# Kernel tuning notes

Measured on AMD Instinct MI355X. Metric: run time of the kernel, lower is better.

Reference implementation:

```python
import jax, jax.numpy as jnp
import numpy as np

N_PROT, N_SUB = 50000, 2000
D_PROT, D_SUB, D_PROJ, KERNEL, N_INT = 256, 256, 128, 16, 64


def setup_inputs() -> dict:
    key = jax.random.key(0)
    ks = jax.random.split(key, 8)
    init = lambda k, shape: jax.random.normal(k, shape, dtype=jnp.float32) * 0.02
    return {
        "prot_node": jax.random.normal(ks[0], (N_PROT, D_PROT), dtype=jnp.float32),
        "sub_node": jax.random.normal(ks[1], (N_SUB, D_SUB), dtype=jnp.float32),
        "int_index": jax.random.randint(ks[2], (N_INT,), 0, N_SUB),
        "Wp": init(ks[3], (D_PROT, D_PROJ)),  # prot_proj weight (in,out layout)
        "bp": jnp.zeros((D_PROJ,), jnp.float32),
        "Ws": init(ks[4], (D_SUB, D_PROJ)),   # sub_proj weight
        "bs": jnp.zeros((D_PROJ,), jnp.float32),
        "wa": init(ks[5], (2 * D_PROJ,)),     # attention_proj weight (out dim 1)
        "ba": jnp.zeros((), jnp.float32),
        "sub_out": init(ks[6], (D_PROJ, D_SUB)),
        "prot_out": init(ks[7], (D_PROJ, D_PROT)),
    }


def reference(prot_node, sub_node, int_index, Wp, bp, Ws, bs, wa, ba, sub_out, prot_out):
    K = KERNEL
    prot_proj = prot_node @ Wp + bp                              # [N, D]
    # reaction potion: sum of projected interacting substrate nodes -> [D]
    reaction = jnp.sum(sub_node[int_index] @ Ws + bs, axis=0)
    num_windows = prot_node.shape[0] - K + 1                     # W
    # attention_proj(concat(window_row, reaction)) splits linearly:
    #   logit = window_row . wa[:D] + reaction . wa[D:] + ba
    # The reaction part is a per-row constant -> compute per-node logits once.
    w1, w2 = wa[:D_PROJ], wa[D_PROJ:]
    g = prot_proj @ w1 + (reaction @ w2 + ba)                    # [N]
    # sliding-window gather indices [W, K]
    idx = jnp.arange(num_windows)[:, None] + jnp.arange(K)[None, :]
    attn = jax.nn.softmax(g[idx], axis=1)                        # [W, K] softmax over window
    local = jnp.einsum('wk,wkd->wd', attn, prot_proj[idx])       # [W, D]
    scores = local + reaction                                    # [W, D]
    # rank windows and pick the best
    top = jnp.argmax(jnp.sum(scores, axis=1))
    top_score = scores[top]                                      # [D]
    # scatter updates back into the node features
    # (set matches torch's non-accumulating fancy-index += for duplicate indices;
    #  the added delta is identical for every row anyway)
    sub_new = sub_node.at[int_index].set(sub_node[int_index] + top_score @ sub_out)
    prot_delta = top_score @ prot_out                            # [D_PROT]
    win = jax.lax.dynamic_slice(prot_node, (top, 0), (K, D_PROT))
    prot_new = jax.lax.dynamic_update_slice(prot_node, win + prot_delta, (top, 0))
    return prot_new, sub_new, int_index
```

## Files before the change

kernel.cpp:

```cpp
#include <hip/hip_runtime.h>
#include <math.h>

#define N_PROT 50000
#define N_SUB  2000
#define D_PROT 256
#define D_SUB  256
#define D_PROJ 128
#define KW     16
#define N_INT  64
#define NWIN   (N_PROT - KW + 1)

#define OUT_SUB (N_PROT * D_PROT)
#define OUT_IDX (OUT_SUB + N_SUB * D_SUB)

#define WS_PACK  0
#define WS_REACT 2
#define WS_CNT   130
#define WS_U1    132
#define WS_U2    388
#define WS_G     644
#define WS_P     (WS_G + N_PROT)

#define PB 1563
#define SB 64
#define NBLK (PB + SB)
#define WBLK ((NWIN + 255) / 256)

__global__ __launch_bounds__(256) void k_prep(
    const float* __restrict__ sub_node, const int* __restrict__ int_index,
    const float* __restrict__ Ws, const float* __restrict__ bs,
    const float* __restrict__ Wp, const float* __restrict__ wa,
    float* __restrict__ ws) {
  const int tid = threadIdx.x;
  if (blockIdx.x == 0) {
    __shared__ int   sidx[N_INT];
    __shared__ float ssum[D_SUB];
    if (tid < N_INT) sidx[tid] = int_index[tid];
    __syncthreads();
    float acc = 0.f;
    #pragma unroll 8
    for (int i = 0; i < N_INT; ++i) acc += sub_node[sidx[i] * D_SUB + tid];
    ssum[tid] = acc;
    __syncthreads();
    if (tid < D_PROJ) {
      float r = 64.0f * bs[tid];
      #pragma unroll 8
      for (int d = 0; d < D_SUB; ++d) r = fmaf(ssum[d], Ws[d * D_PROJ + tid], r);
      ws[WS_REACT + tid] = r;
    }
    if (tid == 0) {
      *((unsigned long long*)ws) = 0ull;
      ((unsigned int*)ws)[WS_CNT] = 0u;
    }
  } else {
    __shared__ float swa[D_PROJ];
    if (tid < D_PROJ) swa[tid] = wa[tid];
    __syncthreads();
    float s1 = 0.f, s2 = 0.f;
    const float4* wrow = (const float4*)&Wp[tid * D_PROJ];
    #pragma unroll 8
    for (int j4 = 0; j4 < D_PROJ / 4; ++j4) {
      float4 w = wrow[j4];
      float4 a = *(const float4*)&swa[j4 * 4];
      s1 = fmaf(w.x, a.x, fmaf(w.y, a.y, fmaf(w.z, a.z, fmaf(w.w, a.w, s1))));
      s2 += w.x + w.y + w.z + w.w;
    }
    ws[WS_U1 + tid] = s1;
    ws[WS_U2 + tid] = s2;
  }
}

__global__ __launch_bounds__(256) void k_main(
    const float* __restrict__ prot, const float* __restrict__ sub_node,
    const int* __restrict__ int_index, float* __restrict__ out,
    float* __restrict__ ws) {
  const int tid = threadIdx.x, lane = tid & 63, wave = tid >> 6;
  const int b = blockIdx.x;
  if (b < PB) {
    const float4 c1 = *(const float4*)&ws[WS_U1 + lane * 4];
    const float4 c2 = *(const float4*)&ws[WS_U2 + lane * 4];
    const int rbase = b * 32 + wave * 8;
    if (rbase + 8 <= N_PROT) {
      float4 av[8];
      #pragma unroll
      for (int i = 0; i < 8; ++i)
        av[i] = *(const float4*)&prot[(rbase + i) * D_PROT + lane * 4];
      #pragma unroll
      for (int i = 0; i < 8; ++i)
        *(float4*)&out[(rbase + i) * D_PROT + lane * 4] = av[i];
      #pragma unroll
      for (int i = 0; i < 8; ++i) {
        float g = av[i].x * c1.x + av[i].y * c1.y + av[i].z * c1.z + av[i].w * c1.w;
        float p = av[i].x * c2.x + av[i].y * c2.y + av[i].z * c2.z + av[i].w * c2.w;
        #pragma unroll
        for (int off = 32; off > 0; off >>= 1) {
          g += __shfl_xor(g, off, 64);
          p += __shfl_xor(p, off, 64);
        }
        if (lane == 0) {
          const int r = rbase + i;
          ws[WS_G + r] = g; ws[WS_P + r] = p;
        }
      }
    } else {
      for (int i = 0; i < 8; ++i) {
        const int r = rbase + i;
        if (r >= N_PROT) break;
        const float4 av = *(const float4*)&prot[r * D_PROT + lane * 4];
        *(float4*)&out[r * D_PROT + lane * 4] = av;
        float g = av.x * c1.x + av.y * c1.y + av.z * c1.z + av.w * c1.w;
        float p = av.x * c2.x + av.y * c2.y + av.z * c2.z + av.w * c2.w;
        for (int off = 32; off > 0; off >>= 1) {
          g += __shfl_xor(g, off, 64);
          p += __shfl_xor(p, off, 64);
        }
        if (lane == 0) { ws[WS_G + r] = g; ws[WS_P + r] = p; }
      }
    }
  } else {
    const int sb = b - PB;
    #pragma unroll
    for (int i = 0; i < 8; ++i) {
      const int gi = sb * 2048 + i * 256 + tid;
      if (gi < (N_SUB * D_SUB) / 4)
        *(float4*)&out[OUT_SUB + gi * 4] = *(const float4*)&sub_node[gi * 4];
    }
    if (sb == 0 && tid < N_INT) out[OUT_IDX + tid] = (float)int_index[tid];
  }
}

__global__ __launch_bounds__(256) void k_finish(
    const float* __restrict__ prot, const float* __restrict__ sub_node,
    const int* __restrict__ int_index, const float* __restrict__ Wp,
    const float* __restrict__ bp, const float* __restrict__ sub_out,
    const float* __restrict__ prot_out, float* __restrict__ ws,
    float* __restrict__ out) {
  __shared__ float sg[256 + KW], sp[256 + KW];
  __shared__ unsigned long long wred[4];
  __shared__ int slast;
  const int tid = threadIdx.x;
  const int w0 = blockIdx.x * 256;
  for (int i = tid; i < 256 + KW - 1; i += 256) {
    int idx = w0 + i;
    bool ok = idx < N_PROT;
    sg[i] = ok ? ws[WS_G + idx] : -1e30f;
    sp[i] = ok ? ws[WS_P + idx] : 0.f;
  }
  __syncthreads();
  {
    int w = w0 + tid;
    unsigned long long best = 0ull;
    if (w < NWIN) {
      float m = sg[tid];
      #pragma unroll
      for (int k = 1; k < KW; ++k) m = fmaxf(m, sg[tid + k]);
      float s = 0.f, t = 0.f;
      #pragma unroll
      for (int k = 0; k < KW; ++k) {
        float e = expf(sg[tid + k] - m);
        s += e;
        t = fmaf(e, sp[tid + k], t);
      }
      t /= s;
      unsigned int bb = __float_as_uint(t);
      unsigned int u = bb ^ ((bb & 0x80000000u) ? 0xFFFFFFFFu : 0x80000000u);
      best = ((unsigned long long)u << 32) |
             (unsigned long long)(0xFFFFFFFFu - (unsigned)w);
    }
    #pragma unroll
    for (int off = 32; off > 0; off >>= 1) {
      unsigned long long o = __shfl_xor(best, off, 64);
      if (o > best) best = o;
    }
    if ((tid & 63) == 0) wred[tid >> 6] = best;
  }
  __syncthreads();
  if (tid == 0) {
    unsigned long long b2 = wred[0];
    for (int i = 1; i < 4; ++i) if (wred[i] > b2) b2 = wred[i];
    atomicMax((unsigned long long*)ws, b2);
    __threadfence();
    unsigned int ticket = atomicAdd(&((unsigned int*)ws)[WS_CNT], 1u);
    slast = (ticket == WBLK - 1) ? 1 : 0;
  }
  __syncthreads();
  if (!slast) return;

  __shared__ float aprot[KW][D_PROT];
  __shared__ float proj16[KW][D_PROJ];
  __shared__ float attn[KW];
  __shared__ float ts[D_PROJ];
  __shared__ float pdelta[D_PROT], sdelta[D_SUB];
  __shared__ int   sidx[N_INT];
  __shared__ int   swtop;
  if (tid == 0) {
    unsigned long long pk = atomicMax((unsigned long long*)ws, 0ull);
    swtop = (int)(0xFFFFFFFFu - (unsigned)(pk & 0xFFFFFFFFull));
  }
  __syncthreads();
  const int wtop = swtop;
  if (tid < N_INT) sidx[tid] = int_index[tid];
  for (int i = tid; i < KW * D_PROT; i += 256) {
    int rr = i >> 8, dd = i & 255;
    aprot[rr][dd] = prot[(wtop + rr) * D_PROT + dd];
  }
  __syncthreads();
  const int j = tid & 127, half = tid >> 7;
  float accr[8];
  #pragma unroll
  for (int rr = 0; rr < 8; ++rr) accr[rr] = bp[j];
  for (int k = 0; k < D_PROT; ++k) {
    float wv = Wp[k * D_PROJ + j];
    #pragma unroll
    for (int rr = 0; rr < 8; ++rr)
      accr[rr] = fmaf(aprot[half * 8 + rr][k], wv, accr[rr]);
  }
  #pragma unroll
  for (int rr = 0; rr < 8; ++rr) proj16[half * 8 + rr][j] = accr[rr];
  __syncthreads();
  if (tid == 0) {
    float m = ws[WS_G + wtop];
    for (int k = 1; k < KW; ++k) m = fmaxf(m, ws[WS_G + wtop + k]);
    float e[KW], s = 0.f;
    for (int k = 0; k < KW; ++k) { e[k] = expf(ws[WS_G + wtop + k] - m); s += e[k]; }
    for (int k = 0; k < KW; ++k) attn[k] = e[k] / s;
  }
  __syncthreads();
  if (tid < D_PROJ) {
    float a = ws[WS_REACT + tid];
    #pragma unroll
    for (int k = 0; k < KW; ++k) a = fmaf(attn[k], proj16[k][tid], a);
    ts[tid] = a;
  }
  __syncthreads();
  {
    float pa = 0.f, sa = 0.f;
    #pragma unroll 8
    for (int jj = 0; jj < D_PROJ; ++jj) {
      float t = ts[jj];
      pa = fmaf(t, prot_out[jj * D_PROT + tid], pa);
      sa = fmaf(t, sub_out[jj * D_SUB + tid], sa);
    }
    pdelta[tid] = pa; sdelta[tid] = sa;
  }
  __syncthreads();
  for (int i = tid; i < KW * D_PROT; i += 256) {
    int rr = i >> 8, dd = i & 255;
    out[(wtop + rr) * D_PROT + dd] = aprot[rr][dd] + pdelta[dd];
  }
  for (int i = 0; i < N_INT; ++i) {
    int idx = sidx[i];
    out[OUT_SUB + idx * D_SUB + tid] = sub_node[idx * D_SUB + tid] + sdelta[tid];
  }
}

extern "C" void kernel_launch(void* const* d_in, const int* in_sizes, int n_in,
                              void* d_out, int out_size, void* d_ws, size_t ws_size,
                              hipStream_t stream) {
  const float* prot     = (const float*)d_in[0];
  const float* sub      = (const float*)d_in[1];
  const int*   idx      = (const int*)d_in[2];
  const float* Wp       = (const float*)d_in[3];
  const float* bp       = (const float*)d_in[4];
  const float* Ws       = (const float*)d_in[5];
  const float* bs       = (const float*)d_in[6];
  const float* wa       = (const float*)d_in[7];
  const float* sub_out  = (const float*)d_in[9];
  const float* prot_out = (const float*)d_in[10];
  float* out = (float*)d_out;
  float* ws  = (float*)d_ws;

  k_prep<<<2, 256, 0, stream>>>(sub, idx, Ws, bs, Wp, wa, ws);
  k_main<<<NBLK, 256, 0, stream>>>(prot, sub, idx, out, ws);
  k_finish<<<WBLK, 256, 0, stream>>>(prot, sub, idx, Wp, bp, sub_out, prot_out,
                                     ws, out);
}
```

Before: 178.0 us.

## Reorder top-window projection as attention-weighted GEMV and widen finish blocks to 1024

The finish kernel now first forms the attention-weighted sum of the top window's raw protein rows and projects only that vector through Wp. This replaces projecting all 16 rows, relying on the attention weights summing to one so the bias is added once. Blocks grow to 1024 threads, so there are fewer blocks and atomics in the window scan, and the serial tail work is spread across more threads with vectorized float4 loads and stores. Larger blocks may lower occupancy in the scan phase, and summation order changes slightly.

```diff
diff --git a/kernel.cpp b/kernel.cpp
--- a/kernel.cpp
+++ b/kernel.cpp
@@ -24,7 +24,7 @@
 #define PB 1563
 #define SB 64
 #define NBLK (PB + SB)
-#define WBLK ((NWIN + 255) / 256)
+#define WBLK ((NWIN + 1023) / 1024)
 
 __global__ __launch_bounds__(256) void k_prep(
     const float* __restrict__ sub_node, const int* __restrict__ int_index,
@@ -129,18 +129,18 @@
   }
 }
 
-__global__ __launch_bounds__(256) void k_finish(
+__global__ __launch_bounds__(1024) void k_finish(
     const float* __restrict__ prot, const float* __restrict__ sub_node,
     const int* __restrict__ int_index, const float* __restrict__ Wp,
     const float* __restrict__ bp, const float* __restrict__ sub_out,
     const float* __restrict__ prot_out, float* __restrict__ ws,
     float* __restrict__ out) {
-  __shared__ float sg[256 + KW], sp[256 + KW];
-  __shared__ unsigned long long wred[4];
+  __shared__ float sg[1024 + KW], sp[1024 + KW];
+  __shared__ unsigned long long wred[16];
   __shared__ int slast;
   const int tid = threadIdx.x;
-  const int w0 = blockIdx.x * 256;
-  for (int i = tid; i < 256 + KW - 1; i += 256) {
+  const int w0 = blockIdx.x * 1024;
+  for (int i = tid; i < 1024 + KW - 1; i += 1024) {
     int idx = w0 + i;
     bool ok = idx < N_PROT;
     sg[i] = ok ? ws[WS_G + idx] : -1e30f;
@@ -177,7 +177,7 @@
   __syncthreads();
   if (tid == 0) {
     unsigned long long b2 = wred[0];
-    for (int i = 1; i < 4; ++i) if (wred[i] > b2) b2 = wred[i];
+    for (int i = 1; i < 16; ++i) if (wred[i] > b2) b2 = wred[i];
     atomicMax((unsigned long long*)ws, b2);
     __threadfence();
     unsigned int ticket = atomicAdd(&((unsigned int*)ws)[WS_CNT], 1u);
@@ -187,9 +187,11 @@
   if (!slast) return;
 
   __shared__ float aprot[KW][D_PROT];
-  __shared__ float proj16[KW][D_PROJ];
   __shared__ float attn[KW];
+  __shared__ float v[D_PROT];
+  __shared__ float part[8][D_PROJ];
   __shared__ float ts[D_PROJ];
+  __shared__ float partP[4][D_PROT], partS[4][D_PROT];
   __shared__ float pdelta[D_PROT], sdelta[D_SUB];
   __shared__ int   sidx[N_INT];
   __shared__ int   swtop;
@@ -199,25 +201,11 @@
   }
   __syncthreads();
   const int wtop = swtop;
+  {
+    const int row = tid >> 6, c4 = (tid & 63) * 4;
+    *(float4*)&aprot[row][c4] = *(const float4*)&prot[(wtop + row) * D_PROT + c4];
+  }
   if (tid < N_INT) sidx[tid] = int_index[tid];
-  for (int i = tid; i < KW * D_PROT; i += 256) {
-    int rr = i >> 8, dd = i & 255;
-    aprot[rr][dd] = prot[(wtop + rr) * D_PROT + dd];
-  }
-  __syncthreads();
-  const int j = tid & 127, half = tid >> 7;
-  float accr[8];
-  #pragma unroll
-  for (int rr = 0; rr < 8; ++rr) accr[rr] = bp[j];
-  for (int k = 0; k < D_PROT; ++k) {
-    float wv = Wp[k * D_PROJ + j];
-    #pragma unroll
-    for (int rr = 0; rr < 8; ++rr)
-      accr[rr] = fmaf(aprot[half * 8 + rr][k], wv, accr[rr]);
-  }
-  #pragma unroll
-  for (int rr = 0; rr < 8; ++rr) proj16[half * 8 + rr][j] = accr[rr];
-  __syncthreads();
   if (tid == 0) {
     float m = ws[WS_G + wtop];
     for (int k = 1; k < KW; ++k) m = fmaxf(m, ws[WS_G + wtop + k]);
@@ -226,31 +214,62 @@
     for (int k = 0; k < KW; ++k) attn[k] = e[k] / s;
   }
   __syncthreads();
+  if (tid < D_PROT) {
+    float a = 0.f;
+    #pragma unroll
+    for (int k = 0; k < KW; ++k) a = fmaf(attn[k], aprot[k][tid], a);
+    v[tid] = a;
+  }
+  __syncthreads();
+  {
+    const int j = tid & 127, s = tid >> 7;
+    float p = 0.f;
+    const float* wp = Wp + (s * 32) * D_PROJ + j;
+    #pragma unroll 8
+    for (int d = 0; d < 32; ++d) p = fmaf(v[s * 32 + d], wp[d * D_PROJ], p);
+    part[s][j] = p;
+  }
+  __syncthreads();
   if (tid < D_PROJ) {
-    float a = ws[WS_REACT + tid];
-    #pragma unroll
-    for (int k = 0; k < KW; ++k) a = fmaf(attn[k], proj16[k][tid], a);
+    float a = ws[WS_REACT + tid] + bp[tid];
+    #pragma unroll
+    for (int s = 0; s < 8; ++s) a += part[s][tid];
     ts[tid] = a;
   }
   __syncthreads();
   {
-    float pa = 0.f, sa = 0.f;
-    #pragma unroll 8
-    for (int jj = 0; jj < D_PROJ; ++jj) {
-      float t = ts[jj];
-      pa = fmaf(t, prot_out[jj * D_PROT + tid], pa);
-      sa = fmaf(t, sub_out[jj * D_SUB + tid], sa);
-    }
-    pdelta[tid] = pa; sdelta[tid] = sa;
-  }
-  __syncthreads();
-  for (int i = tid; i < KW * D_PROT; i += 256) {
-    int rr = i >> 8, dd = i & 255;
-    out[(wtop + rr) * D_PROT + dd] = aprot[rr][dd] + pdelta[dd];
-  }
-  for (int i = 0; i < N_INT; ++i) {
-    int idx = sidx[i];
-    out[OUT_SUB + idx * D_SUB + tid] = sub_node[idx * D_SUB + tid] + sdelta[tid];
+    const int d = tid & 255, s = tid >> 8;
+    float pp = 0.f, ss = 0.f;
+    #pragma unroll 8
+    for (int j = 0; j < 32; ++j) {
+      const float t = ts[s * 32 + j];
+      pp = fmaf(t, prot_out[(s * 32 + j) * D_PROT + d], pp);
+      ss = fmaf(t, sub_out[(s * 32 + j) * D_SUB + d], ss);
+    }
+    partP[s][d] = pp; partS[s][d] = ss;
+  }
+  __syncthreads();
+  if (tid < D_PROT) {
+    pdelta[tid] = partP[0][tid] + partP[1][tid] + partP[2][tid] + partP[3][tid];
+    sdelta[tid] = partS[0][tid] + partS[1][tid] + partS[2][tid] + partS[3][tid];
+  }
+  __syncthreads();
+  {
+    const int row = tid >> 6, c4 = (tid & 63) * 4;
+    float4 a = *(float4*)&aprot[row][c4];
+    float4 d = *(float4*)&pdelta[c4];
+    a.x += d.x; a.y += d.y; a.z += d.z; a.w += d.w;
+    *(float4*)&out[(wtop + row) * D_PROT + c4] = a;
+  }
+  #pragma unroll
+  for (int it = 0; it < 4; ++it) {
+    const int f = tid + it * 1024;
+    const int row = f >> 6, c4 = (f & 63) * 4;
+    const int rr = sidx[row];
+    float4 sv = *(const float4*)&sub_node[rr * D_SUB + c4];
+    float4 d = *(float4*)&sdelta[c4];
+    sv.x += d.x; sv.y += d.y; sv.z += d.z; sv.w += d.w;
+    *(float4*)&out[OUT_SUB + rr * D_SUB + c4] = sv;
   }
 }
 
@@ -272,6 +291,6 @@
 
   k_prep<<<2, 256, 0, stream>>>(sub, idx, Ws, bs, Wp, wa, ws);
   k_main<<<NBLK, 256, 0, stream>>>(prot, sub, idx, out, ws);
-  k_finish<<<WBLK, 256, 0, stream>>>(prot, sub, idx, Wp, bp, sub_out, prot_out,
-                                     ws, out);
-}
+  k_finish<<<WBLK, 1024, 0, stream>>>(prot, sub, idx, Wp, bp, sub_out, prot_out,
+                                      ws, out);
+}
```

After: 151.3 us. 1.18x faster.
